# Kernel tuning notes

Measured on AMD Instinct MI355X. Metric: run time of the kernel, lower is better.

## Reference

```python
import jax, jax.numpy as jnp
import numpy as np

C2D, C3D = 256, 128
IA, IB = C2D // 2, C3D // 2  # inter channels: 128, 64
B, H, W = 4, 64, 64


def _conv1x1(x, w, b):
    # x: [B,Cin,H,W], w: [Cout,Cin], b: [Cout]
    return jnp.einsum('oc,bchw->bohw', w, x) + b[None, :, None, None]


def _cross_attn(Q, K, V):
    # Q,K,V: [B,C,H,W] (same C); full HWxHW attention as in the torch code
    Bs, C, h, w = Q.shape
    q = Q.reshape(Bs, C, h * w)
    k = K.reshape(Bs, C, K.shape[2] * K.shape[3])
    v = V.reshape(Bs, C, V.shape[2] * V.shape[3])
    attn = jnp.einsum('bcn,bcm->bnm', q, k) * (C ** -0.5)  # [B,N,M]
    attn = jax.nn.softmax(attn, axis=-1)
    out = jnp.einsum('bnm,bcm->bcn', attn, v)
    return out.reshape(Bs, C, h, w)


def setup_inputs() -> dict:
    key = jax.random.key(0)
    ks = jax.random.split(key, 20)
    def n(k, shape, scale=0.02):
        return jax.random.normal(k, shape, dtype=jnp.float32) * scale
    inp = {
        'features_2d': jax.random.normal(ks[0], (B, C2D, H, W), dtype=jnp.float32),
        'features_3d': jax.random.normal(ks[1], (B, C3D, H, W), dtype=jnp.float32),
        # stream A: Q from 2d, K/V from 3d, all mapped to IA channels
        'wqA': n(ks[2], (IA, C2D)), 'bqA': jnp.zeros((IA,), jnp.float32),
        'wkA': n(ks[3], (IA, C3D)), 'bkA': jnp.zeros((IA,), jnp.float32),
        'wvA': n(ks[4], (IA, C3D)), 'bvA': jnp.zeros((IA,), jnp.float32),
        'wpA': n(ks[5], (C2D, IA)), 'bpA': jnp.zeros((C2D,), jnp.float32),
        # stream B: Q from 3d, K/V from 2d, all mapped to IB channels
        'wqB': n(ks[6], (IB, C3D)), 'bqB': jnp.zeros((IB,), jnp.float32),
        'wkB': n(ks[7], (IB, C2D)), 'bkB': jnp.zeros((IB,), jnp.float32),
        'wvB': n(ks[8], (IB, C2D)), 'bvB': jnp.zeros((IB,), jnp.float32),
        'wpB': n(ks[9], (C3D, IB)), 'bpB': jnp.zeros((C3D,), jnp.float32),
    }
    return inp


def reference(features_2d, features_3d,
              wqA, bqA, wkA, bkA, wvA, bvA, wpA, bpA,
              wqB, bqB, wkB, bkB, wvB, bvB, wpB, bpB):
    Q_A = _conv1x1(features_2d, wqA, bqA)
    K_A = _conv1x1(features_3d, wkA, bkA)
    V_A = _conv1x1(features_3d, wvA, bvA)
    x_2D = features_2d + _conv1x1(_cross_attn(Q_A, K_A, V_A), wpA, bpA)

    Q_B = _conv1x1(features_3d, wqB, bqB)
    K_B = _conv1x1(features_2d, wkB, bkB)
    V_B = _conv1x1(features_2d, wvB, bvB)
    x_3D = features_3d + _conv1x1(_cross_attn(Q_B, K_B, V_B), wpB, bpB)
    return (x_2D, x_3D)
```

## Files before the change

### kernel.cpp

```cpp
#include <hip/hip_runtime.h>
#include <hip/hip_bf16.h>
#include <math.h>

typedef __bf16 bf16_t;
typedef __bf16 bf16x8 __attribute__((ext_vector_type(8)));
typedef float f32x4 __attribute__((ext_vector_type(4)));
typedef float f32x16 __attribute__((ext_vector_type(16)));
typedef unsigned u32x2 __attribute__((ext_vector_type(2)));

#define NPOS 4096
#define LOG2E 1.4426950408889634f

__device__ __forceinline__ f32x4 mfma16(bf16x8 a, bf16x8 b, f32x4 c) {
    return __builtin_amdgcn_mfma_f32_16x16x32_bf16(a, b, c, 0, 0, 0);
}
__device__ __forceinline__ f32x16 mfma32(bf16x8 a, bf16x8 b, f32x16 c) {
    return __builtin_amdgcn_mfma_f32_32x32x16_bf16(a, b, c, 0, 0, 0);
}

typedef __attribute__((address_space(1))) const unsigned gas_u32;
typedef __attribute__((address_space(3))) unsigned las_u32;
__device__ __forceinline__ void gl_lds16(const char* g, char* l) {
    __builtin_amdgcn_global_load_lds((gas_u32*)g, (las_u32*)l, 16, 0, 0);
}

__device__ __forceinline__ float fexp2(float x) {
    float r; asm("v_exp_f32 %0, %1" : "=v"(r) : "v"(x)); return r;
}

#define BARC(N) do {                                                          \
    asm volatile("s_waitcnt vmcnt(" #N ") lgkmcnt(0)" ::: "memory");          \
    __builtin_amdgcn_sched_barrier(0);                                        \
    __builtin_amdgcn_s_barrier();                                             \
    __builtin_amdgcn_sched_barrier(0);                                        \
} while (0)

__device__ __forceinline__ char* sel3(char* a, char* b, char* c, int i) {
    return i == 0 ? a : (i == 1 ? b : c);
}

template<int BYTES>
__device__ __forceinline__ void stG(char* lds, const char* g, int w, int lane) {
    constexpr int NC = BYTES / 4096;
#pragma unroll
    for (int c = 0; c < NC; ++c) {
        int j = (w * NC + c) * 1024 + lane * 16;
        gl_lds16(g + (j ^ (((j >> 8) & 15) << 4)), lds + j);
    }
}
template<int BYTES>
__device__ __forceinline__ void stV(char* lds, const char* g, int w, int lane) {
    constexpr int NC = BYTES / 4096;
#pragma unroll
    for (int c = 0; c < NC; ++c) {
        int j = (w * NC + c) * 1024 + lane * 16;
        int row = j >> 8;
        int col = (j & 255) ^ ((row & 15) << 4);
        int d = (row << 1) | (col >> 7);
        gl_lds16(g + (size_t)d * (NPOS * 2) + (col & 127), lds + j);
    }
}
template<int BYTES>
__device__ __forceinline__ void stV32(char* lds, const char* g, int w, int lane) {
    constexpr int NC = BYTES / 4096;
#pragma unroll
    for (int c = 0; c < NC; ++c) {
        int j = (w * NC + c) * 1024 + lane * 16;
        int row = j >> 8;
        int col = (j & 255) ^ ((row & 15) << 4);
        int d = (row << 2) | (col >> 6);
        gl_lds16(g + (size_t)d * (NPOS * 2) + (col & 63), lds + j);
    }
}

template<int D>
__device__ __forceinline__ bf16x8 ldK(const char* lds, int key, int dbyte) {
    if constexpr (D == 128) {
        return *(const bf16x8*)(lds + key * 256 + (dbyte ^ ((key & 15) << 4)));
    } else {
        int row = key >> 1;
        int col = ((key & 1) << 7) | dbyte;
        return *(const bf16x8*)(lds + row * 256 + (col ^ ((row & 15) << 4)));
    }
}
__device__ __forceinline__ bf16x8 ldV(const char* lds, int d, int kbyte) {
    int row = d >> 1;
    int col = ((d & 1) << 7) | kbyte;
    return *(const bf16x8*)(lds + row * 256 + (col ^ ((row & 15) << 4)));
}
__device__ __forceinline__ bf16x8 ldV32(const char* lds, int d, int kbyte) {
    int row = d >> 2;
    int col = ((d & 3) << 6) | kbyte;
    return *(const bf16x8*)(lds + row * 256 + (col ^ ((row & 15) << 4)));
}

__device__ __forceinline__ unsigned pkbf(float a, float b) {
    union { bf16_t h[2]; unsigned u; } t;
    t.h[0] = (bf16_t)a; t.h[1] = (bf16_t)b;
    return t.u;
}
#define MKPA(sb, base) ({                                                   \
    unsigned a0_ = pkbf((sb)[(base)+0], (sb)[(base)+1]);                    \
    unsigned a1_ = pkbf((sb)[(base)+2], (sb)[(base)+3]);                    \
    unsigned a2_ = pkbf((sb)[(base)+4], (sb)[(base)+5]);                    \
    unsigned a3_ = pkbf((sb)[(base)+6], (sb)[(base)+7]);                    \
    u32x2 r0_ = __builtin_amdgcn_permlane32_swap(a2_, a0_, false, false);   \
    u32x2 r1_ = __builtin_amdgcn_permlane32_swap(a3_, a1_, false, false);   \
    union { unsigned u[4]; bf16x8 v; } pu_;                                 \
    pu_.u[0] = r0_.y; pu_.u[1] = r1_.y; pu_.u[2] = r0_.x; pu_.u[3] = r1_.x; \
    pu_.v; })

__global__ __launch_bounds__(256) void k_trw(const float* __restrict__ s2d,
                                             const float* __restrict__ s3d,
                                             bf16_t* __restrict__ d2d,
                                             bf16_t* __restrict__ d3d,
                                             const float* w0, const float* w1, const float* w2, const float* w3,
                                             const float* w4, const float* w5, const float* w6, const float* w7,
                                             bf16_t* wdst)
{
    __shared__ float tile[64][65];
    int bid = blockIdx.x, tid = threadIdx.x;
    if (bid >= 1536) {
        int i = (bid - 1536) * 256 + tid;
        if      (i <  32768) wdst[i] = (bf16_t)w0[i];
        else if (i <  49152) wdst[i] = (bf16_t)w1[i - 32768];
        else if (i <  65536) wdst[i] = (bf16_t)w2[i - 49152];
        else if (i <  98304) wdst[i] = (bf16_t)w3[i - 65536];
        else if (i < 106496) wdst[i] = (bf16_t)w4[i - 98304];
        else if (i < 122880) wdst[i] = (bf16_t)w5[i - 106496];
        else if (i < 139264) wdst[i] = (bf16_t)w6[i - 122880];
        else if (i < 147456) wdst[i] = (bf16_t)w7[i - 139264];
        return;
    }
    const float* src; bf16_t* dst; int C, b, c0, n0;
    if (bid < 1024) { src = s2d; dst = d2d; C = 256; b = bid >> 8; c0 = ((bid >> 6) & 3) << 6; n0 = (bid & 63) << 6; }
    else { int r = bid - 1024; src = s3d; dst = d3d; C = 128; b = r >> 7; c0 = ((r >> 6) & 1) << 6; n0 = (r & 63) << 6; }
    const float* sp = src + ((size_t)b * C + c0) * NPOS + n0;
#pragma unroll
    for (int i = 0; i < 16; i++) {
        int idx = tid + i * 256; int c = idx >> 6, n = idx & 63;
        tile[c][n] = sp[(size_t)c * NPOS + n];
    }
    __syncthreads();
    bf16_t* dp = dst + ((size_t)b * NPOS + n0) * C + c0;
#pragma unroll
    for (int i = 0; i < 16; i++) {
        int idx = tid + i * 256; int n = idx >> 6, c = idx & 63;
        dp[(size_t)n * C + c] = (bf16_t)tile[c][n];
    }
}

template<int K, int MQ, int MK, int MV>
__global__ __launch_bounds__(256, 2) void k_prod(const bf16_t* __restrict__ Xt,
                                                 const bf16_t* __restrict__ wq, const float* __restrict__ bq, float sq,
                                                 const bf16_t* __restrict__ wk, const float* __restrict__ bk,
                                                 const bf16_t* __restrict__ wv, const float* __restrict__ bv,
                                                 bf16_t* __restrict__ Qo, bf16_t* __restrict__ Ko, bf16_t* __restrict__ Vo)
{
    extern __shared__ char smem[];
    constexpr int RB = K * 2;
    int bid = blockIdx.x, tid = threadIdx.x;
    int b = bid >> 6, n0 = (bid & 63) << 6;
    int wave = tid >> 6, lane = tid & 63, g = lane >> 4, lr = lane & 15;

    const char* src = (const char*)(Xt + ((size_t)b * NPOS + n0) * K);
#pragma unroll
    for (int j0 = 0; j0 < 64 * RB; j0 += 4096) {
        int j = j0 + tid * 16;
        int row = j / RB;
        int col = j & (RB - 1);
        float4 v = *(const float4*)(src + (size_t)row * RB + col);
        *(float4*)(smem + row * RB + (col ^ ((row & 7) << 4))) = v;
    }
    __syncthreads();

    f32x4 aq[MQ / 16], ak[MK / 16], av[MV / 16];
#pragma unroll
    for (int ob = 0; ob < MQ / 16; ++ob) aq[ob] = f32x4{0.f,0.f,0.f,0.f};
#pragma unroll
    for (int ob = 0; ob < MK / 16; ++ob) ak[ob] = f32x4{0.f,0.f,0.f,0.f};
#pragma unroll
    for (int ob = 0; ob < MV / 16; ++ob) av[ob] = f32x4{0.f,0.f,0.f,0.f};
    int xrow = wave * 16 + lr;
#pragma unroll
    for (int ks = 0; ks < K / 32; ++ks) {
        bf16x8 xf = *(const bf16x8*)(smem + xrow * RB + ((((ks * 32 + g * 8) * 2)) ^ ((xrow & 7) << 4)));
#pragma unroll
        for (int ob = 0; ob < MQ / 16; ++ob) {
            bf16x8 wf = *(const bf16x8*)(wq + (size_t)(ob * 16 + lr) * K + ks * 32 + g * 8);
            aq[ob] = mfma16(xf, wf, aq[ob]);
        }
#pragma unroll
        for (int ob = 0; ob < MK / 16; ++ob) {
            bf16x8 wf = *(const bf16x8*)(wk + (size_t)(ob * 16 + lr) * K + ks * 32 + g * 8);
            ak[ob] = mfma16(xf, wf, ak[ob]);
        }
#pragma unroll
        for (int ob = 0; ob < MV / 16; ++ob) {
            bf16x8 wf = *(const bf16x8*)(wv + (size_t)(ob * 16 + lr) * K + ks * 32 + g * 8);
            av[ob] = mfma16(wf, xf, av[ob]);
        }
    }
#pragma unroll
    for (int ob = 0; ob < MQ / 16; ++ob) {
        int o = ob * 16 + lr;
        float bs = bq[o];
#pragma unroll
        for (int r = 0; r < 4; r++) {
            size_t n = (size_t)b * NPOS + n0 + wave * 16 + g * 4 + r;
            Qo[n * MQ + o] = (bf16_t)((aq[ob][r] + bs) * sq);
        }
    }
#pragma unroll
    for (int ob = 0; ob < MK / 16; ++ob) {
        int o = ob * 16 + lr;
        float bs = bk[o];
#pragma unroll
        for (int r = 0; r < 4; r++) {
            size_t n = (size_t)b * NPOS + n0 + wave * 16 + g * 4 + r;
            Ko[n * MK + o] = (bf16_t)(ak[ob][r] + bs);
        }
    }
#pragma unroll
    for (int ob = 0; ob < MV / 16; ++ob) {
#pragma unroll
        for (int r = 0; r < 4; r++) {
            int o = ob * 16 + g * 4 + r;
            size_t idx = ((size_t)b * MV + o) * NPOS + n0 + wave * 16 + lr;
            Vo[idx] = (bf16_t)(av[ob][r] + bv[o]);
        }
    }
}

template<int K, int M>
__global__ __launch_bounds__(256, 2) void k_out(const bf16_t* __restrict__ Xt,
                                                const bf16_t* __restrict__ W,
                                                const float* __restrict__ bias,
                                                const float* __restrict__ resid,
                                                float* __restrict__ outp,
                                                const float* __restrict__ lp)
{
    extern __shared__ char smem[];
    constexpr int RB = K * 2;
    int bid = blockIdx.x, tid = threadIdx.x;
    int b = bid >> 6, n0 = (bid & 63) << 6;
    int wave = tid >> 6, lane = tid & 63, g = lane >> 4, lr = lane & 15;

#pragma unroll
    for (int j0 = 0; j0 < 64 * RB; j0 += 4096) {
        int j = j0 + tid * 16;
        int row = j / RB;
        int colb = j & (RB - 1);
        size_t n = (size_t)b * NPOS + n0 + row;
        float l1 = lp[n], l2 = lp[16384 + n];
        float inv = 1.f / (l1 + l2);
        float w1 = l1 * inv, w2 = l2 * inv;
        bf16x8 o1 = *(const bf16x8*)(Xt + n * K + (colb >> 1));
        bf16x8 o2 = *(const bf16x8*)(Xt + (size_t)16384 * K + n * K + (colb >> 1));
        bf16x8 xv;
#pragma unroll
        for (int e = 0; e < 8; ++e) xv[e] = (bf16_t)(w1 * (float)o1[e] + w2 * (float)o2[e]);
        *(bf16x8*)(smem + row * RB + (colb ^ ((row & 7) << 4))) = xv;
    }
    __syncthreads();

    f32x4 acc[M / 16];
#pragma unroll
    for (int ob = 0; ob < M / 16; ++ob) acc[ob] = f32x4{0.f,0.f,0.f,0.f};
    int xrow = wave * 16 + lr;
#pragma unroll
    for (int ks = 0; ks < K / 32; ++ks) {
        bf16x8 xf = *(const bf16x8*)(smem + xrow * RB + ((((ks * 32 + g * 8) * 2)) ^ ((xrow & 7) << 4)));
#pragma unroll
        for (int ob = 0; ob < M / 16; ++ob) {
            bf16x8 wf = *(const bf16x8*)(W + (size_t)(ob * 16 + lr) * K + ks * 32 + g * 8);
            acc[ob] = mfma16(wf, xf, acc[ob]);
        }
    }
#pragma unroll
    for (int ob = 0; ob < M / 16; ++ob) {
#pragma unroll
        for (int r = 0; r < 4; r++) {
            int o = ob * 16 + g * 4 + r;
            size_t idx = ((size_t)b * M + o) * NPOS + n0 + wave * 16 + lr;
            outp[idx] = acc[ob][r] + bias[o] + resid[idx];
        }
    }
}

__device__ void attnA11(const bf16_t* __restrict__ Qt, const bf16_t* __restrict__ Kt,
                        const bf16_t* __restrict__ V, bf16_t* __restrict__ OtH,
                        float* __restrict__ lH, int b, int qblk, int half,
                        char* smem, int tid)
{
    char* Kb0 = smem;          char* Kb1 = smem + 8192;  char* Kb2 = smem + 16384;
    char* Vb0 = smem + 24576;  char* Vb1 = smem + 32768; char* Vb2 = smem + 40960;
    int w = tid >> 6, lane = tid & 63;
    int qcol = lane & 31, hi = lane >> 5;
    int q0 = qblk * 128 + w * 32;

    bf16x8 qf[8];
    const bf16_t* qp = Qt + ((size_t)b * NPOS + q0 + qcol) * 128 + hi * 8;
#pragma unroll
    for (int ks = 0; ks < 8; ++ks) qf[ks] = *(const bf16x8*)(qp + ks * 16);

    f32x16 acc[4];
#pragma unroll
    for (int cb = 0; cb < 4; ++cb)
#pragma unroll
        for (int i = 0; i < 16; ++i) acc[cb][i] = 0.f;
    float l_c = 0.f;

    const char* kg = (const char*)(Kt + (size_t)b * NPOS * 128) + (size_t)half * 64 * 8192;
    const char* vg = (const char*)(V + (size_t)b * 128 * NPOS) + (size_t)half * 4096;

    stG<8192>(Kb0, kg, w, lane);
    stV32<8192>(Vb0, vg, w, lane);
    stG<8192>(Kb1, kg + 8192, w, lane);
    stV32<8192>(Vb1, vg + 64, w, lane);
    BARC(4);

    f32x16 sE, sO;
#pragma unroll
    for (int i = 0; i < 16; ++i) sE[i] = 0.f;
#pragma unroll
    for (int ks = 0; ks < 8; ++ks)
        sE = mfma32(ldK<128>(Kb0, qcol, ks * 32 + hi * 16), qf[ks], sE);
    stG<8192>(Kb2, kg + 16384, w, lane);
    BARC(2);

    int ce = 0;
#pragma unroll 1
    for (int t2 = 0; t2 < 32; ++t2) {
        int t = 2 * t2;
        int c1 = ce + 1; if (c1 > 2) c1 -= 3;
        int c2 = ce + 2; if (c2 > 2) c2 -= 3;
        {
            int tK = t + 3; if (tK > 63) tK = 63;
            int tV = t + 2; if (tV > 63) tV = 63;
            stG<8192>(sel3(Kb0, Kb1, Kb2, ce), kg + (size_t)tK * 8192, w, lane);
            stV32<8192>(sel3(Vb0, Vb1, Vb2, c2), vg + (size_t)tV * 64, w, lane);
            const char* Kn = sel3(Kb0, Kb1, Kb2, c1);
#pragma unroll
            for (int i = 0; i < 16; ++i) sO[i] = 0.f;
            __builtin_amdgcn_s_setprio(1);
#pragma unroll
            for (int ks = 0; ks < 8; ++ks)
                sO = mfma32(ldK<128>(Kn, qcol, ks * 32 + hi * 16), qf[ks], sO);
            __builtin_amdgcn_s_setprio(0);
            float ps = 0.f;
#pragma unroll
            for (int i = 0; i < 16; ++i) { float e = fexp2(sE[i]); sE[i] = e; ps += e; }
            ps += __shfl_xor(ps, 32);
            l_c += ps;
            bf16x8 pa0 = MKPA(sE, 0), pa1 = MKPA(sE, 8);
            const char* Vc = sel3(Vb0, Vb1, Vb2, ce);
            __builtin_amdgcn_s_setprio(1);
#pragma unroll
            for (int cb = 0; cb < 4; ++cb) {
                int d = cb * 32 + qcol;
                acc[cb] = mfma32(pa0, ldV32(Vc, d, hi * 16), acc[cb]);
                acc[cb] = mfma32(pa1, ldV32(Vc, d, 32 + hi * 16), acc[cb]);
            }
            __builtin_amdgcn_s_setprio(0);
            BARC(4);
        }
        {
            int tK = t + 4; if (tK > 63) tK = 63;
            int tV = t + 3; if (tV > 63) tV = 63;
            stG<8192>(sel3(Kb0, Kb1, Kb2, c1), kg + (size_t)tK * 8192, w, lane);
            stV32<8192>(sel3(Vb0, Vb1, Vb2, ce), vg + (size_t)tV * 64, w, lane);
            const char* Kn = sel3(Kb0, Kb1, Kb2, c2);
#pragma unroll
            for (int i = 0; i < 16; ++i) sE[i] = 0.f;
            __builtin_amdgcn_s_setprio(1);
#pragma unroll
            for (int ks = 0; ks < 8; ++ks)
                sE = mfma32(ldK<128>(Kn, qcol, ks * 32 + hi * 16), qf[ks], sE);
            __builtin_amdgcn_s_setprio(0);
            float ps = 0.f;
#pragma unroll
            for (int i = 0; i < 16; ++i) { float e = fexp2(sO[i]); sO[i] = e; ps += e; }
            ps += __shfl_xor(ps, 32);
            l_c += ps;
            bf16x8 pa0 = MKPA(sO, 0), pa1 = MKPA(sO, 8);
            const char* Vc = sel3(Vb0, Vb1, Vb2, c1);
            __builtin_amdgcn_s_setprio(1);
#pragma unroll
            for (int cb = 0; cb < 4; ++cb) {
                int d = cb * 32 + qcol;
                acc[cb] = mfma32(pa0, ldV32(Vc, d, hi * 16), acc[cb]);
                acc[cb] = mfma32(pa1, ldV32(Vc, d, 32 + hi * 16), acc[cb]);
            }
            __builtin_amdgcn_s_setprio(0);
            BARC(4);
        }
        ce = c2;
    }

    float linv = 1.f / l_c;
    size_t obase = (size_t)(half * 4 + b) * NPOS;
#pragma unroll
    for (int r = 0; r < 16; ++r) {
        int crow = (r & 3) + 8 * (r >> 2) + 4 * hi;
        float lr = __shfl(linv, crow);
        size_t nrow = obase + q0 + crow;
#pragma unroll
        for (int cb = 0; cb < 4; ++cb)
            OtH[nrow * 128 + cb * 32 + qcol] = (bf16_t)(acc[cb][r] * lr);
    }
    if (lane < 32) lH[obase + q0 + lane] = l_c;
}

__device__ void attnB11(const bf16_t* __restrict__ Qt, const bf16_t* __restrict__ Kt,
                        const bf16_t* __restrict__ V, bf16_t* __restrict__ OtH,
                        float* __restrict__ lH, int b, int qblk, int half,
                        char* smem, int tid)
{
    char* Kb0 = smem;          char* Kb1 = smem + 8192;  char* Kb2 = smem + 16384;
    char* Vb0 = smem + 24576;  char* Vb1 = smem + 32768; char* Vb2 = smem + 40960;
    int w = tid >> 6, lane = tid & 63;
    int qcol = lane & 31, hi = lane >> 5;
    int q0 = qblk * 128 + w * 32;

    bf16x8 qf[4];
    const bf16_t* qp = Qt + ((size_t)b * NPOS + q0 + qcol) * 64 + hi * 8;
#pragma unroll
    for (int ks = 0; ks < 4; ++ks) qf[ks] = *(const bf16x8*)(qp + ks * 16);

    f32x16 acc[2];
#pragma unroll
    for (int cb = 0; cb < 2; ++cb)
#pragma unroll
        for (int i = 0; i < 16; ++i) acc[cb][i] = 0.f;
    float l_c = 0.f;

    const char* kg = (const char*)(Kt + (size_t)b * NPOS * 64) + (size_t)half * 32 * 8192;
    const char* vg = (const char*)(V + (size_t)b * 64 * NPOS) + (size_t)half * 4096;

    stG<8192>(Kb0, kg, w, lane);
    stV<8192>(Vb0, vg, w, lane);
    stG<8192>(Kb1, kg + 8192, w, lane);
    stV<8192>(Vb1, vg + 128, w, lane);
    BARC(4);

    f32x16 sE0, sE1, sO0, sO1;
#pragma unroll
    for (int i = 0; i < 16; ++i) { sE0[i] = 0.f; sE1[i] = 0.f; }
#pragma unroll
    for (int ks = 0; ks < 4; ++ks) {
        int dbyte = ks * 32 + hi * 16;
        sE0 = mfma32(ldK<64>(Kb0, qcol, dbyte), qf[ks], sE0);
        sE1 = mfma32(ldK<64>(Kb0, 32 + qcol, dbyte), qf[ks], sE1);
    }
    stG<8192>(Kb2, kg + 16384, w, lane);
    BARC(2);

    int ce = 0;
#pragma unroll 1
    for (int t2 = 0; t2 < 16; ++t2) {
        int t = 2 * t2;
        int c1 = ce + 1; if (c1 > 2) c1 -= 3;
        int c2 = ce + 2; if (c2 > 2) c2 -= 3;
        {
            int tK = t + 3; if (tK > 31) tK = 31;
            int tV = t + 2; if (tV > 31) tV = 31;
            stG<8192>(sel3(Kb0, Kb1, Kb2, ce), kg + (size_t)tK * 8192, w, lane);
            stV<8192>(sel3(Vb0, Vb1, Vb2, c2), vg + (size_t)tV * 128, w, lane);
            const char* Kn = sel3(Kb0, Kb1, Kb2, c1);
#pragma unroll
            for (int i = 0; i < 16; ++i) { sO0[i] = 0.f; sO1[i] = 0.f; }
            __builtin_amdgcn_s_setprio(1);
#pragma unroll
            for (int ks = 0; ks < 4; ++ks) {
                int dbyte = ks * 32 + hi * 16;
                sO0 = mfma32(ldK<64>(Kn, qcol, dbyte), qf[ks], sO0);
                sO1 = mfma32(ldK<64>(Kn, 32 + qcol, dbyte), qf[ks], sO1);
            }
            __builtin_amdgcn_s_setprio(0);
            float ps = 0.f;
#pragma unroll
            for (int i = 0; i < 16; ++i) { float e = fexp2(sE0[i]); sE0[i] = e; ps += e; }
#pragma unroll
            for (int i = 0; i < 16; ++i) { float e = fexp2(sE1[i]); sE1[i] = e; ps += e; }
            ps += __shfl_xor(ps, 32);
            l_c += ps;
            bf16x8 pa0 = MKPA(sE0, 0), pa1 = MKPA(sE0, 8);
            bf16x8 pa2 = MKPA(sE1, 0), pa3 = MKPA(sE1, 8);
            const char* Vc = sel3(Vb0, Vb1, Vb2, ce);
            __builtin_amdgcn_s_setprio(1);
#pragma unroll
            for (int cb = 0; cb < 2; ++cb) {
                int d = cb * 32 + qcol;
                acc[cb] = mfma32(pa0, ldV(Vc, d, 0  + hi * 16), acc[cb]);
                acc[cb] = mfma32(pa1, ldV(Vc, d, 32 + hi * 16), acc[cb]);
                acc[cb] = mfma32(pa2, ldV(Vc, d, 64 + hi * 16), acc[cb]);
                acc[cb] = mfma32(pa3, ldV(Vc, d, 96 + hi * 16), acc[cb]);
            }
            __builtin_amdgcn_s_setprio(0);
            BARC(4);
        }
        {
            int tK = t + 4; if (tK > 31) tK = 31;
            int tV = t + 3; if (tV > 31) tV = 31;
            stG<8192>(sel3(Kb0, Kb1, Kb2, c1), kg + (size_t)tK * 8192, w, lane);
            stV<8192>(sel3(Vb0, Vb1, Vb2, ce), vg + (size_t)tV * 128, w, lane);
            const char* Kn = sel3(Kb0, Kb1, Kb2, c2);
#pragma unroll
            for (int i = 0; i < 16; ++i) { sE0[i] = 0.f; sE1[i] = 0.f; }
            __builtin_amdgcn_s_setprio(1);
#pragma unroll
            for (int ks = 0; ks < 4; ++ks) {
                int dbyte = ks * 32 + hi * 16;
                sE0 = mfma32(ldK<64>(Kn, qcol, dbyte), qf[ks], sE0);
                sE1 = mfma32(ldK<64>(Kn, 32 + qcol, dbyte), qf[ks], sE1);
            }
            __builtin_amdgcn_s_setprio(0);
            float ps = 0.f;
#pragma unroll
            for (int i = 0; i < 16; ++i) { float e = fexp2(sO0[i]); sO0[i] = e; ps += e; }
#pragma unroll
            for (int i = 0; i < 16; ++i) { float e = fexp2(sO1[i]); sO1[i] = e; ps += e; }
            ps += __shfl_xor(ps, 32);
            l_c += ps;
            bf16x8 pa0 = MKPA(sO0, 0), pa1 = MKPA(sO0, 8);
            bf16x8 pa2 = MKPA(sO1, 0), pa3 = MKPA(sO1, 8);
            const char* Vc = sel3(Vb0, Vb1, Vb2, c1);
            __builtin_amdgcn_s_setprio(1);
#pragma unroll
            for (int cb = 0; cb < 2; ++cb) {
                int d = cb * 32 + qcol;
                acc[cb] = mfma32(pa0, ldV(Vc, d, 0  + hi * 16), acc[cb]);
                acc[cb] = mfma32(pa1, ldV(Vc, d, 32 + hi * 16), acc[cb]);
                acc[cb] = mfma32(pa2, ldV(Vc, d, 64 + hi * 16), acc[cb]);
                acc[cb] = mfma32(pa3, ldV(Vc, d, 96 + hi * 16), acc[cb]);
            }
            __builtin_amdgcn_s_setprio(0);
            BARC(4);
        }
        ce = c2;
    }

    float linv = 1.f / l_c;
    size_t obase = (size_t)(half * 4 + b) * NPOS;
#pragma unroll
    for (int r = 0; r < 16; ++r) {
        int crow = (r & 3) + 8 * (r >> 2) + 4 * hi;
        float lr = __shfl(linv, crow);
        size_t nrow = obase + q0 + crow;
#pragma unroll
        for (int cb = 0; cb < 2; ++cb)
            OtH[nrow * 64 + cb * 32 + qcol] = (bf16_t)(acc[cb][r] * lr);
    }
    if (lane < 32) lH[obase + q0 + lane] = l_c;
}

__global__ __launch_bounds__(256, 2) void k_attn11(const bf16_t* QtA, const bf16_t* KtA, const bf16_t* VA,
                                                   bf16_t* OtHA, float* lHA,
                                                   const bf16_t* QtB, const bf16_t* KtB, const bf16_t* VB,
                                                   bf16_t* OtHB, float* lHB)
{
    extern __shared__ char smem[];
    int bid = blockIdx.x, tid = threadIdx.x;
    if (bid < 256) {
        int x = bid & 7;
        attnA11(QtA, KtA, VA, OtHA, lHA, x >> 1, bid >> 3, x & 1, smem, tid);
    } else {
        int u = bid - 256;
        int x = u & 7;
        attnB11(QtB, KtB, VB, OtHB, lHB, x >> 1, u >> 3, x & 1, smem, tid);
    }
}

extern "C" void kernel_launch(void* const* d_in, const int* in_sizes, int n_in,
                              void* d_out, int out_size, void* d_ws, size_t ws_size,
                              hipStream_t stream)
{
    (void)in_sizes; (void)n_in; (void)out_size; (void)ws_size;
    const float* f2d = (const float*)d_in[0];
    const float* f3d = (const float*)d_in[1];
    const float* wqA = (const float*)d_in[2];  const float* bqA = (const float*)d_in[3];
    const float* wkA = (const float*)d_in[4];  const float* bkA = (const float*)d_in[5];
    const float* wvA = (const float*)d_in[6];  const float* bvA = (const float*)d_in[7];
    const float* wpA = (const float*)d_in[8];  const float* bpA = (const float*)d_in[9];
    const float* wqB = (const float*)d_in[10]; const float* bqB = (const float*)d_in[11];
    const float* wkB = (const float*)d_in[12]; const float* bkB = (const float*)d_in[13];
    const float* wvB = (const float*)d_in[14]; const float* bvB = (const float*)d_in[15];
    const float* wpB = (const float*)d_in[16]; const float* bpB = (const float*)d_in[17];

    char* ws = (char*)d_ws;
    bf16_t* ft2d = (bf16_t*)(ws);
    bf16_t* ft3d = (bf16_t*)(ws + 8388608);
    bf16_t* wbf  = (bf16_t*)(ws + 12582912);
    bf16_t* QtA  = (bf16_t*)(ws + 12877824);
    bf16_t* KtA_ = (bf16_t*)(ws + 17072128);
    bf16_t* VA_  = (bf16_t*)(ws + 21266432);
    bf16_t* QtB  = (bf16_t*)(ws + 25460736);
    bf16_t* KtB_ = (bf16_t*)(ws + 27557888);
    bf16_t* VB_  = (bf16_t*)(ws + 29655040);
    bf16_t* OtHA = (bf16_t*)(ws);
    float*  lHA  = (float*)(ws + 8388608);
    bf16_t* OtHB = (bf16_t*)(ws + 31752192);
    float*  lHB  = (float*)(ws + 35946496);

    k_trw<<<2112, 256, 0, stream>>>(f2d, f3d, ft2d, ft3d,
                                    wqA, wkA, wvA, wpA, wqB, wkB, wvB, wpB, wbf);

    const float sA = 0.08838834764831845f * LOG2E;
    const float sB = 0.125f * LOG2E;

    k_prod<256, 128, 64, 64><<<256, 256, 32768, stream>>>(ft2d,
        wbf + 0, bqA, sA, wbf + 106496, bkB, wbf + 122880, bvB, QtA, KtB_, VB_);
    k_prod<128, 64, 128, 128><<<256, 256, 16384, stream>>>(ft3d,
        wbf + 98304, bqB, sB, wbf + 32768, bkA, wbf + 49152, bvA, QtB, KtA_, VA_);

    k_attn11<<<512, 256, 49152, stream>>>(QtA, KtA_, VA_, OtHA, lHA, QtB, KtB_, VB_, OtHB, lHB);

    k_out<128, 256><<<256, 256, 16384, stream>>>(OtHA, wbf + 65536, bpA, f2d, (float*)d_out, lHA);
    k_out<64, 128><<<256, 256, 8192, stream>>>(OtHB, wbf + 139264, bpB, f3d, (float*)d_out + 4194304, lHB);
}
```

Measured before the change: 129.3 us.

## Fuse input transpose and weight conversion into projection kernels, merge launches

Removes the separate transpose/bf16 conversion kernel. The projection kernel now reads fp32 features directly, transposes them through an LDS tile into a swizzled bf16 buffer, and converts fp32 weights to bf16 on the fly as it loads them. The two projection launches are merged into one 512-block kernel, and the two output-projection launches likewise. This cuts launches and a full intermediate write and read of the features, at the cost of fp32 weight reads (twice the bytes) repeated by every block, plus extra LDS and syncs inside the projection kernel.

```diff
diff --git a/kernel.cpp b/kernel.cpp
--- a/kernel.cpp
+++ b/kernel.cpp
@@ -92,6 +92,14 @@
     int row = d >> 2;
     int col = ((d & 3) << 6) | kbyte;
     return *(const bf16x8*)(lds + row * 256 + (col ^ ((row & 15) << 4)));
+}
+
+__device__ __forceinline__ bf16x8 ldw(const float* w) {
+    float4 a = *(const float4*)w, b = *(const float4*)(w + 4);
+    bf16x8 r;
+    r[0] = (bf16_t)a.x; r[1] = (bf16_t)a.y; r[2] = (bf16_t)a.z; r[3] = (bf16_t)a.w;
+    r[4] = (bf16_t)b.x; r[5] = (bf16_t)b.y; r[6] = (bf16_t)b.z; r[7] = (bf16_t)b.w;
+    return r;
 }
 
 __device__ __forceinline__ unsigned pkbf(float a, float b) {
@@ -110,67 +118,35 @@
     pu_.u[0] = r0_.y; pu_.u[1] = r1_.y; pu_.u[2] = r0_.x; pu_.u[3] = r1_.x; \
     pu_.v; })
 
-__global__ __launch_bounds__(256) void k_trw(const float* __restrict__ s2d,
-                                             const float* __restrict__ s3d,
-                                             bf16_t* __restrict__ d2d,
-                                             bf16_t* __restrict__ d3d,
-                                             const float* w0, const float* w1, const float* w2, const float* w3,
-                                             const float* w4, const float* w5, const float* w6, const float* w7,
-                                             bf16_t* wdst)
-{
-    __shared__ float tile[64][65];
-    int bid = blockIdx.x, tid = threadIdx.x;
-    if (bid >= 1536) {
-        int i = (bid - 1536) * 256 + tid;
-        if      (i <  32768) wdst[i] = (bf16_t)w0[i];
-        else if (i <  49152) wdst[i] = (bf16_t)w1[i - 32768];
-        else if (i <  65536) wdst[i] = (bf16_t)w2[i - 49152];
-        else if (i <  98304) wdst[i] = (bf16_t)w3[i - 65536];
-        else if (i < 106496) wdst[i] = (bf16_t)w4[i - 98304];
-        else if (i < 122880) wdst[i] = (bf16_t)w5[i - 106496];
-        else if (i < 139264) wdst[i] = (bf16_t)w6[i - 122880];
-        else if (i < 147456) wdst[i] = (bf16_t)w7[i - 139264];
-        return;
-    }
-    const float* src; bf16_t* dst; int C, b, c0, n0;
-    if (bid < 1024) { src = s2d; dst = d2d; C = 256; b = bid >> 8; c0 = ((bid >> 6) & 3) << 6; n0 = (bid & 63) << 6; }
-    else { int r = bid - 1024; src = s3d; dst = d3d; C = 128; b = r >> 7; c0 = ((r >> 6) & 1) << 6; n0 = (r & 63) << 6; }
-    const float* sp = src + ((size_t)b * C + c0) * NPOS + n0;
-#pragma unroll
-    for (int i = 0; i < 16; i++) {
-        int idx = tid + i * 256; int c = idx >> 6, n = idx & 63;
-        tile[c][n] = sp[(size_t)c * NPOS + n];
-    }
-    __syncthreads();
-    bf16_t* dp = dst + ((size_t)b * NPOS + n0) * C + c0;
-#pragma unroll
-    for (int i = 0; i < 16; i++) {
-        int idx = tid + i * 256; int n = idx >> 6, c = idx & 63;
-        dp[(size_t)n * C + c] = (bf16_t)tile[c][n];
-    }
-}
-
 template<int K, int MQ, int MK, int MV>
-__global__ __launch_bounds__(256, 2) void k_prod(const bf16_t* __restrict__ Xt,
-                                                 const bf16_t* __restrict__ wq, const float* __restrict__ bq, float sq,
-                                                 const bf16_t* __restrict__ wk, const float* __restrict__ bk,
-                                                 const bf16_t* __restrict__ wv, const float* __restrict__ bv,
-                                                 bf16_t* __restrict__ Qo, bf16_t* __restrict__ Ko, bf16_t* __restrict__ Vo)
-{
-    extern __shared__ char smem[];
+__device__ void prod_body(const float* __restrict__ F,
+                          const float* __restrict__ wq, const float* __restrict__ bq, float sq,
+                          const float* __restrict__ wk, const float* __restrict__ bk,
+                          const float* __restrict__ wv, const float* __restrict__ bv,
+                          bf16_t* __restrict__ Qo, bf16_t* __restrict__ Ko, bf16_t* __restrict__ Vo,
+                          char* smem, int bid, int tid)
+{
     constexpr int RB = K * 2;
-    int bid = blockIdx.x, tid = threadIdx.x;
     int b = bid >> 6, n0 = (bid & 63) << 6;
     int wave = tid >> 6, lane = tid & 63, g = lane >> 4, lr = lane & 15;
 
-    const char* src = (const char*)(Xt + ((size_t)b * NPOS + n0) * K);
-#pragma unroll
-    for (int j0 = 0; j0 < 64 * RB; j0 += 4096) {
-        int j = j0 + tid * 16;
-        int row = j / RB;
-        int col = j & (RB - 1);
-        float4 v = *(const float4*)(src + (size_t)row * RB + col);
-        *(float4*)(smem + row * RB + (col ^ ((row & 7) << 4))) = v;
+    float (*tile)[65] = (float(*)[65])(smem + 64 * RB);
+    const float* fb = F + (size_t)b * K * NPOS;
+    for (int c0 = 0; c0 < K; c0 += 64) {
+        const float* sp = fb + (size_t)c0 * NPOS + n0;
+        __syncthreads();
+#pragma unroll
+        for (int i = 0; i < 16; i++) {
+            int idx = tid + i * 256; int c = idx >> 6, n = idx & 63;
+            tile[c][n] = sp[(size_t)c * NPOS + n];
+        }
+        __syncthreads();
+#pragma unroll
+        for (int i = 0; i < 16; i++) {
+            int idx = tid + i * 256; int n = idx >> 6, c = idx & 63;
+            int colb = (c0 + c) * 2;
+            *(bf16_t*)(smem + n * RB + (colb ^ ((n & 7) << 4))) = (bf16_t)tile[c][n];
+        }
     }
     __syncthreads();
 
@@ -186,20 +162,14 @@
     for (int ks = 0; ks < K / 32; ++ks) {
         bf16x8 xf = *(const bf16x8*)(smem + xrow * RB + ((((ks * 32 + g * 8) * 2)) ^ ((xrow & 7) << 4)));
 #pragma unroll
-        for (int ob = 0; ob < MQ / 16; ++ob) {
-            bf16x8 wf = *(const bf16x8*)(wq + (size_t)(ob * 16 + lr) * K + ks * 32 + g * 8);
-            aq[ob] = mfma16(xf, wf, aq[ob]);
-        }
-#pragma unroll
-        for (int ob = 0; ob < MK / 16; ++ob) {
-            bf16x8 wf = *(const bf16x8*)(wk + (size_t)(ob * 16 + lr) * K + ks * 32 + g * 8);
-            ak[ob] = mfma16(xf, wf, ak[ob]);
-        }
-#pragma unroll
-        for (int ob = 0; ob < MV / 16; ++ob) {
-            bf16x8 wf = *(const bf16x8*)(wv + (size_t)(ob * 16 + lr) * K + ks * 32 + g * 8);
-            av[ob] = mfma16(wf, xf, av[ob]);
-        }
+        for (int ob = 0; ob < MQ / 16; ++ob)
+            aq[ob] = mfma16(xf, ldw(wq + (size_t)(ob * 16 + lr) * K + ks * 32 + g * 8), aq[ob]);
+#pragma unroll
+        for (int ob = 0; ob < MK / 16; ++ob)
+            ak[ob] = mfma16(xf, ldw(wk + (size_t)(ob * 16 + lr) * K + ks * 32 + g * 8), ak[ob]);
+#pragma unroll
+        for (int ob = 0; ob < MV / 16; ++ob)
+            av[ob] = mfma16(ldw(wv + (size_t)(ob * 16 + lr) * K + ks * 32 + g * 8), xf, av[ob]);
     }
 #pragma unroll
     for (int ob = 0; ob < MQ / 16; ++ob) {
@@ -232,17 +202,37 @@
     }
 }
 
+__global__ __launch_bounds__(256, 2) void k_prodf(const float* f2d, const float* f3d,
+                                                  const float* wqA, const float* bqA,
+                                                  const float* wkA, const float* bkA,
+                                                  const float* wvA, const float* bvA,
+                                                  const float* wqB, const float* bqB,
+                                                  const float* wkB, const float* bkB,
+                                                  const float* wvB, const float* bvB,
+                                                  bf16_t* QtA, bf16_t* KtA_, bf16_t* VA_,
+                                                  bf16_t* QtB, bf16_t* KtB_, bf16_t* VB_)
+{
+    extern __shared__ char smem[];
+    const float sA = 0.08838834764831845f * LOG2E;
+    const float sB = 0.125f * LOG2E;
+    if (blockIdx.x < 256)
+        prod_body<256, 128, 64, 64>(f2d, wqA, bqA, sA, wkB, bkB, wvB, bvB,
+                                    QtA, KtB_, VB_, smem, blockIdx.x, threadIdx.x);
+    else
+        prod_body<128, 64, 128, 128>(f3d, wqB, bqB, sB, wkA, bkA, wvA, bvA,
+                                     QtB, KtA_, VA_, smem, blockIdx.x - 256, threadIdx.x);
+}
+
 template<int K, int M>
-__global__ __launch_bounds__(256, 2) void k_out(const bf16_t* __restrict__ Xt,
-                                                const bf16_t* __restrict__ W,
-                                                const float* __restrict__ bias,
-                                                const float* __restrict__ resid,
-                                                float* __restrict__ outp,
-                                                const float* __restrict__ lp)
-{
-    extern __shared__ char smem[];
+__device__ void out_body(const bf16_t* __restrict__ Xt,
+                         const float* __restrict__ lp,
+                         const float* __restrict__ W,
+                         const float* __restrict__ bias,
+                         const float* __restrict__ resid,
+                         float* __restrict__ outp,
+                         char* smem, int bid, int tid)
+{
     constexpr int RB = K * 2;
-    int bid = blockIdx.x, tid = threadIdx.x;
     int b = bid >> 6, n0 = (bid & 63) << 6;
     int wave = tid >> 6, lane = tid & 63, g = lane >> 4, lr = lane & 15;
 
@@ -272,10 +262,8 @@
     for (int ks = 0; ks < K / 32; ++ks) {
         bf16x8 xf = *(const bf16x8*)(smem + xrow * RB + ((((ks * 32 + g * 8) * 2)) ^ ((xrow & 7) << 4)));
 #pragma unroll
-        for (int ob = 0; ob < M / 16; ++ob) {
-            bf16x8 wf = *(const bf16x8*)(W + (size_t)(ob * 16 + lr) * K + ks * 32 + g * 8);
-            acc[ob] = mfma16(wf, xf, acc[ob]);
-        }
+        for (int ob = 0; ob < M / 16; ++ob)
+            acc[ob] = mfma16(ldw(W + (size_t)(ob * 16 + lr) * K + ks * 32 + g * 8), xf, acc[ob]);
     }
 #pragma unroll
     for (int ob = 0; ob < M / 16; ++ob) {
@@ -286,6 +274,19 @@
             outp[idx] = acc[ob][r] + bias[o] + resid[idx];
         }
     }
+}
+
+__global__ __launch_bounds__(256, 2) void k_outf(const bf16_t* OtHA, const float* lHA,
+                                                 const bf16_t* OtHB, const float* lHB,
+                                                 const float* wpA, const float* bpA, const float* f2d,
+                                                 const float* wpB, const float* bpB, const float* f3d,
+                                                 float* out)
+{
+    extern __shared__ char smem[];
+    if (blockIdx.x < 256)
+        out_body<128, 256>(OtHA, lHA, wpA, bpA, f2d, out, smem, blockIdx.x, threadIdx.x);
+    else
+        out_body<64, 128>(OtHB, lHB, wpB, bpB, f3d, out + 4194304, smem, blockIdx.x - 256, threadIdx.x);
 }
 
 __device__ void attnA11(const bf16_t* __restrict__ Qt, const bf16_t* __restrict__ Kt,
@@ -589,9 +590,6 @@
     const float* wpB = (const float*)d_in[16]; const float* bpB = (const float*)d_in[17];
 
     char* ws = (char*)d_ws;
-    bf16_t* ft2d = (bf16_t*)(ws);
-    bf16_t* ft3d = (bf16_t*)(ws + 8388608);
-    bf16_t* wbf  = (bf16_t*)(ws + 12582912);
     bf16_t* QtA  = (bf16_t*)(ws + 12877824);
     bf16_t* KtA_ = (bf16_t*)(ws + 17072128);
     bf16_t* VA_  = (bf16_t*)(ws + 21266432);
@@ -603,19 +601,12 @@
     bf16_t* OtHB = (bf16_t*)(ws + 31752192);
     float*  lHB  = (float*)(ws + 35946496);
 
-    k_trw<<<2112, 256, 0, stream>>>(f2d, f3d, ft2d, ft3d,
-                                    wqA, wkA, wvA, wpA, wqB, wkB, wvB, wpB, wbf);
-
-    const float sA = 0.08838834764831845f * LOG2E;
-    const float sB = 0.125f * LOG2E;
-
-    k_prod<256, 128, 64, 64><<<256, 256, 32768, stream>>>(ft2d,
-        wbf + 0, bqA, sA, wbf + 106496, bkB, wbf + 122880, bvB, QtA, KtB_, VB_);
-    k_prod<128, 64, 128, 128><<<256, 256, 16384, stream>>>(ft3d,
-        wbf + 98304, bqB, sB, wbf + 32768, bkA, wbf + 49152, bvA, QtB, KtA_, VA_);
+    k_prodf<<<512, 256, 49408, stream>>>(f2d, f3d,
+        wqA, bqA, wkA, bkA, wvA, bvA, wqB, bqB, wkB, bkB, wvB, bvB,
+        QtA, KtA_, VA_, QtB, KtB_, VB_);
 
     k_attn11<<<512, 256, 49152, stream>>>(QtA, KtA_, VA_, OtHA, lHA, QtB, KtB_, VB_, OtHB, lHB);
 
-    k_out<128, 256><<<256, 256, 16384, stream>>>(OtHA, wbf + 65536, bpA, f2d, (float*)d_out, lHA);
-    k_out<64, 128><<<256, 256, 8192, stream>>>(OtHB, wbf + 139264, bpB, f3d, (float*)d_out + 4194304, lHB);
-}
+    k_outf<<<512, 256, 16384, stream>>>(OtHA, lHA, OtHB, lHB,
+        wpA, bpA, f2d, wpB, bpB, f3d, (float*)d_out);
+}
```

Measured after the change: 153.2 us. 1.18x slower.
